# Optimization experiments

Measured on AMD Instinct MI355X. Metric: run time of the kernel, lower is better.

## Reference

```python
import jax, jax.numpy as jnp
import numpy as np

B = 1; IMG = 256; P = 16; INC = 3; C = 384; NH = 12; HD = C // NH
WS = 8; SH = WS // 2; HP = IMG // P; L = HP * HP; NW = (HP // WS) ** 2
NB = 12; OC = 4; EPS = 1e-5; MLP = 4 * C


def _rel_index(w):
    coords = np.stack(np.meshgrid(np.arange(w), np.arange(w), indexing='ij'))
    cf = coords.reshape(2, -1)
    rel = (cf[:, :, None] - cf[:, None, :]).transpose(1, 2, 0)
    rel[:, :, 0] += w - 1
    rel[:, :, 1] += w - 1
    rel[:, :, 0] *= 2 * w - 1
    return rel.sum(-1)  # (w*w, w*w)


def _attn_mask():
    m = np.zeros((HP, HP))
    cnt = 0
    for hs in (slice(0, -WS), slice(-WS, -SH), slice(-SH, None)):
        for ws_ in (slice(0, -WS), slice(-WS, -SH), slice(-SH, None)):
            m[hs, ws_] = cnt
            cnt += 1
    mw = m.reshape(HP // WS, WS, HP // WS, WS).transpose(0, 2, 1, 3).reshape(-1, WS * WS)
    d = mw[:, None, :] - mw[:, :, None]
    return np.where(d != 0, -100.0, 0.0).astype(np.float32)  # (NW, 64, 64)

_REL_IDX = jnp.asarray(_rel_index(WS))
_AMASK = jnp.asarray(_attn_mask())


def _ln(x, w, b):
    m = jnp.mean(x, -1, keepdims=True)
    d = x - m
    v = jnp.mean(d * d, -1, keepdims=True)
    return d * jax.lax.rsqrt(v + EPS) * w + b


def _resize_ac(x, oh, ow):
    # bilinear, align_corners=True
    H, W = x.shape[-2], x.shape[-1]
    def idx(o, n):
        s = jnp.linspace(0.0, n - 1.0, o)
        i0 = jnp.floor(s).astype(jnp.int32)
        i1 = jnp.minimum(i0 + 1, n - 1)
        return i0, i1, (s - i0.astype(s.dtype)).astype(x.dtype)
    y0, y1, wy = idx(oh, H)
    x0, x1, wx = idx(ow, W)
    r = x[..., y0, :] * (1 - wy)[:, None] + x[..., y1, :] * wy[:, None]
    return r[..., x0] * (1 - wx) + r[..., x1] * wx


def setup_inputs():
    key = jax.random.key(0)
    ks = jax.random.split(key, 16)
    f32 = jnp.float32
    def rn(k, shape, s=0.02):
        return jax.random.normal(k, shape, dtype=f32) * s
    return {
        'x': jax.random.normal(ks[0], (B, INC, IMG, IMG), f32),
        'patch_w': rn(ks[1], (C, INC, P, P), 0.05),
        'patch_b': jnp.zeros((C,), f32),
        'pos_embed': rn(ks[2], (1, L, C)),
        'ln1_w': jnp.ones((NB, C), f32), 'ln1_b': jnp.zeros((NB, C), f32),
        'qkv_w': rn(ks[3], (NB, 3 * C, C)),
        'proj_w': rn(ks[4], (NB, C, C)), 'proj_b': jnp.zeros((NB, C), f32),
        'rpb': rn(ks[5], (NB, (2 * WS - 1) ** 2, NH)),
        'ln2_w': jnp.ones((NB, C), f32), 'ln2_b': jnp.zeros((NB, C), f32),
        'fc1_w': rn(ks[6], (NB, MLP, C)), 'fc1_b': jnp.zeros((NB, MLP), f32),
        'fc2_w': rn(ks[7], (NB, C, MLP)), 'fc2_b': jnp.zeros((NB, C), f32),
        'skip_w': rn(ks[8], (OC, C), 0.05), 'skip_b': jnp.zeros((OC,), f32),
        'dt1_w': rn(ks[9], (C, INC, P, P), 0.05), 'dt1_b': jnp.zeros((INC,), f32),
        'bn1_w': jnp.ones((INC,), f32), 'bn1_b': jnp.zeros((INC,), f32),
        'dt2_w': rn(ks[10], (INC, OC, P, P), 0.05), 'dt2_b': jnp.zeros((OC,), f32),
        'bn2_w': jnp.ones((OC,), f32), 'bn2_b': jnp.zeros((OC,), f32),
    }


def reference(x, patch_w, patch_b, pos_embed, ln1_w, ln1_b, qkv_w, proj_w, proj_b,
              rpb, ln2_w, ln2_b, fc1_w, fc1_b, fc2_w, fc2_b, skip_w, skip_b,
              dt1_w, dt1_b, bn1_w, bn1_b, dt2_w, dt2_b, bn2_w, bn2_b):
    scale = HD ** -0.5
    # --- patch embed (conv k=P, s=P) ---
    xr = x.reshape(B, INC, HP, P, HP, P)
    f = jnp.einsum('bchpwq,ocpq->bohw', xr, patch_w) + patch_b[None, :, None, None]
    # --- buggy token flatten, replicated exactly from the source ---
    t = jnp.transpose(f.reshape(B, C, P, HP // P, P, HP // P), (0, 3, 5, 1, 2, 4)).reshape(B, L, C)
    t = t + pos_embed

    def block(h, p):
        l1w, l1b, qw, pw, pb, rt, l2w, l2b, f1w, f1b, f2w, f2b = p
        sc = h
        y = _ln(h, l1w, l1b).reshape(B, HP, HP, C)
        y = jnp.roll(y, (-SH, -SH), axis=(1, 2))  # every block is shifted in this model
        yw = y.reshape(B, HP // WS, WS, HP // WS, WS, C).transpose(0, 1, 3, 2, 4, 5)
        yw = yw.reshape(B * NW, WS * WS, C)
        qkv = (yw @ qw.T).reshape(B * NW, WS * WS, 3, NH, HD).transpose(2, 0, 3, 1, 4)
        q, k, v = qkv[0], qkv[1], qkv[2]
        attn = jnp.einsum('wnid,wnjd->wnij', q, k) * scale
        bias = rt[_REL_IDX].transpose(2, 0, 1)  # (NH, 64, 64)
        attn = attn + bias[None]
        attn = attn.reshape(B, NW, NH, WS * WS, WS * WS) + _AMASK[None, :, None]
        attn = jax.nn.softmax(attn.reshape(B * NW, NH, WS * WS, WS * WS), axis=-1)
        o = jnp.einsum('wnij,wnjd->wnid', attn, v).transpose(0, 2, 1, 3).reshape(B * NW, WS * WS, C)
        o = o @ pw.T + pb
        o = o.reshape(B, HP // WS, HP // WS, WS, WS, C).transpose(0, 1, 3, 2, 4, 5).reshape(B, HP, HP, C)
        o = jnp.roll(o, (SH, SH), axis=(1, 2)).reshape(B, L, C)
        h = sc + o
        z = _ln(h, l2w, l2b)
        z = jax.nn.gelu(z @ f1w.T + f1b, approximate=False)
        h = h + (z @ f2w.T + f2b)
        return h, None

    t, _ = jax.lax.scan(block, t, (ln1_w, ln1_b, qkv_w, proj_w, proj_b, rpb,
                                   ln2_w, ln2_b, fc1_w, fc1_b, fc2_w, fc2_b))

    f = t.reshape(B, HP, HP, C).transpose(0, 3, 1, 2)  # (B, C, 16, 16)
    # --- decoder ---
    skip = jnp.einsum('bchw,oc->bohw', f, skip_w) + skip_b[None, :, None, None]
    # interpolate(skip, size=(H, W)) with H, W == skip's own size: identity.
    d = jnp.einsum('bchw,cokl->bohkwl', f, dt1_w).reshape(B, INC, HP * P, HP * P) + dt1_b[None, :, None, None]
    d = jax.nn.relu(d / jnp.sqrt(1.0 + EPS) * bn1_w[None, :, None, None] + bn1_b[None, :, None, None])
    d = jnp.einsum('bchw,cokl->bohkwl', d, dt2_w).reshape(B, OC, HP * P * P, HP * P * P) + dt2_b[None, :, None, None]
    d = d / jnp.sqrt(1.0 + EPS) * bn2_w[None, :, None, None] + bn2_b[None, :, None, None]
    # Upsample(scale_factor = IMG // (P*P) = 1): identity.
    skip_up = _resize_ac(skip, d.shape[2], d.shape[3])
    out = (d + skip_up).reshape(B, -1, IMG, IMG)
    return out
```

## Files before the change

### kernel.cpp

```cpp
#include <hip/hip_runtime.h>
#include <cmath>

typedef _Float16 v8h __attribute__((ext_vector_type(8)));
typedef float v4f __attribute__((ext_vector_type(4)));

#define DEV __device__ __forceinline__

DEV int win_map(int m) {
  int w = m >> 6, tok = m & 63;
  int r = ((w >> 1) * 8 + (tok >> 3) + 4) & 15;
  int c = ((w & 1) * 8 + (tok & 7) + 4) & 15;
  return r * 16 + c;
}

template<int MAP>
DEV float4 loadA4(const float* __restrict__ A, int m, int k, int K) {
  if constexpr (MAP == 0) {
    return *(const float4*)(A + (size_t)m * K + k);
  } else if constexpr (MAP == 1) {
    return *(const float4*)(A + (size_t)win_map(m) * 384 + k);
  } else {
    int h = m >> 4, w = m & 15;
    int inc = k >> 8, rem = k & 255, p = rem >> 4, q = rem & 15;
    return *(const float4*)(A + inc * 65536 + (h * 16 + p) * 256 + w * 16 + q);
  }
}

template<int WAVES_M, int WAVES_N, int WN, int MAP, bool LN, int EPI>
__launch_bounds__(256)
__global__ void mgemm(const float* __restrict__ A, const float* __restrict__ W,
                      const float* __restrict__ bias,
                      const float* __restrict__ lnw, const float* __restrict__ lnb,
                      const float* __restrict__ resid, const float* __restrict__ aux,
                      float* __restrict__ Cout, int N, int K) {
  constexpr int BM = WAVES_M * 16;
  constexpr int BN = WAVES_N * WN * 16;
  constexpr int BK = 64;
  constexpr int BKP = BK + 8;

  __shared__ _Float16 As[BM][BKP];
  __shared__ _Float16 Ws[BN][BKP];
  __shared__ float redS[256], redQ[256];
  __shared__ float lmean[BM], lrstd[BM];

  const int t = threadIdx.x;
  const int wave = t >> 6, lane = t & 63;
  const int m0 = blockIdx.y * BM, n0 = blockIdx.x * BN;

  if constexpr (LN) {
    constexpr int PARTS = 256 / BM;
    int r = t / PARTS, part = t % PARTS;
    int chunk = K / PARTS;
    float s = 0.f, sq = 0.f;
    for (int k = part * chunk; k < (part + 1) * chunk; k += 4) {
      float4 v = loadA4<MAP>(A, m0 + r, k, K);
      s += v.x + v.y + v.z + v.w;
      sq += v.x * v.x + v.y * v.y + v.z * v.z + v.w * v.w;
    }
    redS[t] = s; redQ[t] = sq;
    __syncthreads();
    if (t < BM) {
      float ss = 0.f, qq = 0.f;
      for (int p = 0; p < PARTS; ++p) { ss += redS[t * PARTS + p]; qq += redQ[t * PARTS + p]; }
      float mean = ss / K;
      float var = qq / K - mean * mean;
      lmean[t] = mean;
      lrstd[t] = rsqrtf(var + 1e-5f);
    }
    __syncthreads();
  }

  const int wm = wave % WAVES_M;
  const int wn = wave / WAVES_M;
  const int mBase = wm * 16;
  const int nBase = wn * (WN * 16);

  v4f acc[WN] = {};

  for (int k0 = 0; k0 < K; k0 += BK) {
    constexpr int AREP = (BM * 16) / 256;
#pragma unroll
    for (int i = 0; i < AREP; ++i) {
      int idx = t + i * 256;
      int row = idx >> 4;
      int kc = (idx & 15) * 4;
      float4 v = loadA4<MAP>(A, m0 + row, k0 + kc, K);
      if constexpr (LN) {
        float4 lw = *(const float4*)(lnw + k0 + kc);
        float4 lb = *(const float4*)(lnb + k0 + kc);
        float mu = lmean[row], rs = lrstd[row];
        v.x = (v.x - mu) * rs * lw.x + lb.x;
        v.y = (v.y - mu) * rs * lw.y + lb.y;
        v.z = (v.z - mu) * rs * lw.z + lb.z;
        v.w = (v.w - mu) * rs * lw.w + lb.w;
      }
      _Float16* dst = &As[row][kc];
      dst[0] = (_Float16)v.x; dst[1] = (_Float16)v.y;
      dst[2] = (_Float16)v.z; dst[3] = (_Float16)v.w;
    }
    constexpr int WREP = (BN * 16) / 256;
#pragma unroll
    for (int i = 0; i < WREP; ++i) {
      int idx = t + i * 256;
      int row = idx >> 4;
      int kc = (idx & 15) * 4;
      float4 v = *(const float4*)(W + (size_t)(n0 + row) * K + k0 + kc);
      _Float16* dst = &Ws[row][kc];
      dst[0] = (_Float16)v.x; dst[1] = (_Float16)v.y;
      dst[2] = (_Float16)v.z; dst[3] = (_Float16)v.w;
    }
    __syncthreads();
#pragma unroll
    for (int kk = 0; kk < BK; kk += 32) {
      v8h af = *(const v8h*)&As[mBase + (lane & 15)][kk + (lane >> 4) * 8];
#pragma unroll
      for (int nt = 0; nt < WN; ++nt) {
        v8h bf = *(const v8h*)&Ws[nBase + nt * 16 + (lane & 15)][kk + (lane >> 4) * 8];
        acc[nt] = __builtin_amdgcn_mfma_f32_16x16x32_f16(af, bf, acc[nt], 0, 0, 0);
      }
    }
    __syncthreads();
  }

  const int quad = lane >> 4;
  const int col = lane & 15;
#pragma unroll
  for (int nt = 0; nt < WN; ++nt) {
    int n = n0 + nBase + nt * 16 + col;
#pragma unroll
    for (int r = 0; r < 4; ++r) {
      int m = m0 + mBase + quad * 4 + r;
      float v = acc[nt][r];
      if constexpr (EPI == 0) {
        Cout[(size_t)m * N + n] = v;
      } else if constexpr (EPI == 1) {
        Cout[(size_t)m * N + n] = resid[(size_t)m * N + n] + v + bias[n];
      } else if constexpr (EPI == 2) {
        float z = v + bias[n];
        Cout[(size_t)m * N + n] = 0.5f * z * (1.0f + erff(z * 0.70710678118654752f));
      } else {
        Cout[n * 256 + m] = v + bias[n] + aux[n * 256 + m];
      }
    }
  }
}

__launch_bounds__(256)
__global__ void attn_k(const float* __restrict__ qkv, const float* __restrict__ rpb,
                       float* __restrict__ obuf) {
  __shared__ float qs[64][33], ks[64][33], vs[64][33];
  __shared__ float ps[64][68];
  __shared__ float rbias[225];
  __shared__ int labv[64];
  const int t = threadIdx.x;
  const int w = blockIdx.x & 3, head = blockIdx.x >> 2;

  for (int idx = t; idx < 2048; idx += 256) {
    int tok = idx >> 5, d = idx & 31;
    int base = (w * 64 + tok) * 1152 + head * 32 + d;
    qs[tok][d] = qkv[base];
    ks[tok][d] = qkv[base + 384];
    vs[tok][d] = qkv[base + 768];
  }
  for (int idx = t; idx < 225; idx += 256) rbias[idx] = rpb[idx * 12 + head];
  if (t < 64) {
    int r = (w >> 1) * 8 + (t >> 3), c = (w & 1) * 8 + (t & 7);
    int lr = r < 8 ? 0 : (r < 12 ? 1 : 2);
    int lc = c < 8 ? 0 : (c < 12 ? 1 : 2);
    labv[t] = lr * 3 + lc;
  }
  __syncthreads();

  const int tx = t & 15, ty = t >> 4;
  float acc[4][4] = {};
  for (int d = 0; d < 32; ++d) {
    float a[4], b[4];
#pragma unroll
    for (int ii = 0; ii < 4; ++ii) a[ii] = qs[ty * 4 + ii][d];
#pragma unroll
    for (int jj = 0; jj < 4; ++jj) b[jj] = ks[tx * 4 + jj][d];
#pragma unroll
    for (int ii = 0; ii < 4; ++ii)
#pragma unroll
      for (int jj = 0; jj < 4; ++jj) acc[ii][jj] += a[ii] * b[jj];
  }
  const float scale = 0.17677669529663687f;
#pragma unroll
  for (int ii = 0; ii < 4; ++ii) {
    int i = ty * 4 + ii;
    int yi = i >> 3, xi = i & 7, li = labv[i];
    float pv[4];
    float mx = -1e30f;
#pragma unroll
    for (int jj = 0; jj < 4; ++jj) {
      int j = tx * 4 + jj;
      int yj = j >> 3, xj = j & 7;
      int ri = (yi - yj + 7) * 15 + (xi - xj + 7);
      float s = acc[ii][jj] * scale + rbias[ri] + (li == labv[j] ? 0.f : -100.f);
      pv[jj] = s;
      mx = fmaxf(mx, s);
    }
    for (int off = 1; off < 16; off <<= 1) mx = fmaxf(mx, __shfl_xor(mx, off));
    float sum = 0.f;
#pragma unroll
    for (int jj = 0; jj < 4; ++jj) { pv[jj] = expf(pv[jj] - mx); sum += pv[jj]; }
    for (int off = 1; off < 16; off <<= 1) sum += __shfl_xor(sum, off);
    float inv = 1.0f / sum;
#pragma unroll
    for (int jj = 0; jj < 4; ++jj) ps[i][tx * 4 + jj] = pv[jj] * inv;
  }
  __syncthreads();

  float o2[4][2] = {};
  for (int j = 0; j < 64; ++j) {
    float v0 = vs[j][tx * 2 + 0], v1 = vs[j][tx * 2 + 1];
#pragma unroll
    for (int ii = 0; ii < 4; ++ii) {
      float p = ps[ty * 4 + ii][j];
      o2[ii][0] += p * v0;
      o2[ii][1] += p * v1;
    }
  }
#pragma unroll
  for (int ii = 0; ii < 4; ++ii) {
    int l = win_map(w * 64 + ty * 4 + ii);
    obuf[l * 384 + head * 32 + tx * 2 + 0] = o2[ii][0];
    obuf[l * 384 + head * 32 + tx * 2 + 1] = o2[ii][1];
  }
}

__global__ void skip_k(const float* __restrict__ hfin, const float* __restrict__ sw,
                       const float* __restrict__ sb, float* __restrict__ skipb) {
  int o = blockIdx.x, t = threadIdx.x;
  float acc = 0.f;
  for (int c = 0; c < 384; ++c) acc += hfin[t * 384 + c] * sw[o * 384 + c];
  skipb[o * 256 + t] = acc + sb[o];
}

__global__ void d1_k(const float* __restrict__ hfin, const float* __restrict__ wgt,
                     const float* __restrict__ bvec, const float* __restrict__ bnw,
                     const float* __restrict__ bnb, float* __restrict__ d1) {
  __shared__ float hs[2][384];
  const int t = threadIdx.x;
  const int l0 = blockIdx.x * 2;
  for (int idx = t; idx < 768; idx += 256) {
    int pi = idx / 384, c = idx % 384;
    hs[pi][c] = hfin[(l0 + pi) * 384 + c];
  }
  __syncthreads();
  const float invs = rsqrtf(1.0f + 1e-5f);
  const int kk = t >> 4, ll = t & 15;
  for (int o = 0; o < 3; ++o) {
    float a0 = 0.f, a1 = 0.f;
    for (int c = 0; c < 384; ++c) {
      float wv = wgt[c * 768 + o * 256 + t];
      a0 += hs[0][c] * wv;
      a1 += hs[1][c] * wv;
    }
    float sw = bnw[o] * invs, bb = bvec[o], sb = bnb[o];
    float v0 = fmaxf((a0 + bb) * sw + sb, 0.f);
    float v1 = fmaxf((a1 + bb) * sw + sb, 0.f);
#pragma unroll
    for (int pi = 0; pi < 2; ++pi) {
      int l = l0 + pi;
      int h = l >> 4, wq = l & 15;
      float v = pi ? v1 : v0;
      d1[o * 65536 + (h * 16 + kk) * 256 + (wq * 16 + ll)] = v;
    }
  }
}

__launch_bounds__(256)
__global__ void d2_k(const float* __restrict__ d1, const float* __restrict__ w2,
                     const float* __restrict__ b2, const float* __restrict__ bnw,
                     const float* __restrict__ bnb, const float* __restrict__ skipb,
                     float* __restrict__ out) {
  __shared__ float d1s[3][256];
  __shared__ float wcol[3][16];
  __shared__ float srow[16];
  const int t = threadIdx.x;
  const int y = blockIdx.x, o = blockIdx.y;
  const int h2 = y >> 4, k = y & 15;
  for (int idx = t; idx < 768; idx += 256) {
    int c = idx >> 8, wi = idx & 255;
    d1s[c][wi] = d1[c * 65536 + h2 * 256 + wi];
  }
  if (t < 48) {
    int c = t >> 4, l2 = t & 15;
    wcol[c][l2] = w2[c * 1024 + o * 256 + k * 16 + l2];
  }
  if (t < 16) {
    const float dy = 15.0f / 4095.0f;
    float s = y * dy;
    int y0 = min((int)s, 15);
    int y1 = min(y0 + 1, 15);
    float wy = s - (float)y0;
    float a0 = skipb[o * 256 + y0 * 16 + t];
    float a1 = skipb[o * 256 + y1 * 16 + t];
    srow[t] = a0 + (a1 - a0) * wy;
  }
  __syncthreads();
  const float invs = rsqrtf(1.0f + 1e-5f);
  const float sw = bnw[o] * invs;
  const float base = b2[o] * sw + bnb[o];
  const float dx = 15.0f / 4095.0f;
  const size_t obase = ((size_t)o << 24) + ((size_t)y << 12);
#pragma unroll
  for (int rep = 0; rep < 4; ++rep) {
    int x4 = t + rep * 256;
    int x = x4 * 4;
    int wi = x >> 4;
    int l2b = x & 15;
    float vals[4];
#pragma unroll
    for (int e = 0; e < 4; ++e) {
      int l2 = l2b + e;
      float v = d1s[0][wi] * wcol[0][l2] + d1s[1][wi] * wcol[1][l2] + d1s[2][wi] * wcol[2][l2];
      v = v * sw + base;
      float s = (float)(x + e) * dx;
      int x0 = min((int)s, 15);
      int x1 = min(x0 + 1, 15);
      float wx = s - (float)x0;
      vals[e] = v + srow[x0] + (srow[x1] - srow[x0]) * wx;
    }
    *(float4*)&out[obase + x] = make_float4(vals[0], vals[1], vals[2], vals[3]);
  }
}

extern "C" void kernel_launch(void* const* d_in, const int* in_sizes, int n_in,
                              void* d_out, int out_size, void* d_ws, size_t ws_size,
                              hipStream_t stream) {
  const float* x       = (const float*)d_in[0];
  const float* patch_w = (const float*)d_in[1];
  const float* patch_b = (const float*)d_in[2];
  const float* pos     = (const float*)d_in[3];
  const float* ln1w    = (const float*)d_in[4];
  const float* ln1b    = (const float*)d_in[5];
  const float* qkvw    = (const float*)d_in[6];
  const float* projw   = (const float*)d_in[7];
  const float* projb   = (const float*)d_in[8];
  const float* rpb     = (const float*)d_in[9];
  const float* ln2w    = (const float*)d_in[10];
  const float* ln2b    = (const float*)d_in[11];
  const float* fc1w    = (const float*)d_in[12];
  const float* fc1b    = (const float*)d_in[13];
  const float* fc2w    = (const float*)d_in[14];
  const float* fc2b    = (const float*)d_in[15];
  const float* skipw   = (const float*)d_in[16];
  const float* skipbi  = (const float*)d_in[17];
  const float* dt1w    = (const float*)d_in[18];
  const float* dt1b    = (const float*)d_in[19];
  const float* bn1w    = (const float*)d_in[20];
  const float* bn1b    = (const float*)d_in[21];
  const float* dt2w    = (const float*)d_in[22];
  const float* dt2b    = (const float*)d_in[23];
  const float* bn2w    = (const float*)d_in[24];
  const float* bn2b    = (const float*)d_in[25];
  float* out = (float*)d_out;
  float* ws = (float*)d_ws;

  float* h    = ws;
  float* qkvb = ws + 98304;
  float* obuf = ws + 393216;
  float* zb   = ws + 491520;
  float* d1b  = ws + 884736;
  float* skb  = ws + 1081344;

  mgemm<2, 2, 2, 2, false, 3><<<dim3(6, 8), 256, 0, stream>>>(
      x, patch_w, patch_b, nullptr, nullptr, nullptr, pos, h, 384, 768);

  for (int b = 0; b < 12; ++b) {
    mgemm<2, 2, 2, 1, true, 0><<<dim3(18, 8), 256, 0, stream>>>(
        h, qkvw + (size_t)b * 442368, nullptr, ln1w + b * 384, ln1b + b * 384,
        nullptr, nullptr, qkvb, 1152, 384);
    attn_k<<<48, 256, 0, stream>>>(qkvb, rpb + b * 2700, obuf);
    mgemm<1, 4, 1, 0, false, 1><<<dim3(6, 16), 256, 0, stream>>>(
        obuf, projw + (size_t)b * 147456, projb + b * 384, nullptr, nullptr,
        h, nullptr, h, 384, 384);
    mgemm<2, 2, 2, 0, true, 2><<<dim3(24, 8), 256, 0, stream>>>(
        h, fc1w + (size_t)b * 589824, fc1b + b * 1536, ln2w + b * 384, ln2b + b * 384,
        nullptr, nullptr, zb, 1536, 384);
    mgemm<1, 4, 1, 0, false, 1><<<dim3(6, 16), 256, 0, stream>>>(
        zb, fc2w + (size_t)b * 589824, fc2b + b * 384, nullptr, nullptr,
        h, nullptr, h, 384, 1536);
  }

  skip_k<<<4, 256, 0, stream>>>(h, skipw, skipbi, skb);
  d1_k<<<128, 256, 0, stream>>>(h, dt1w, dt1b, bn1w, bn1b, d1b);
  d2_k<<<dim3(4096, 4), 256, 0, stream>>>(d1b, dt2w, dt2b, bn2w, bn2b, skb, out);
}
```

Before: 1.408 ms.

## Fuse whole forward pass into one persistent kernel with grid barriers

Replaces the sequence of roughly 65 separate kernel launches (patch embed, per-block GEMMs and attention, decoder) with a single persistent kernel of 256 workgroups. Stages are separated by a software grid barrier built on atomics. Each stage loops over its tiles with a grid stride, and shared memory is a union across stages. The intent is to remove launch overhead and inter-kernel gaps, which dominate for these small GEMMs. The cost is atomic spin-wait barriers, with a deadlock risk if all 256 workgroups are not co-resident, and fewer parallel blocks in the large decoder stage.

```diff
diff --git a/kernel.cpp b/kernel.cpp
--- a/kernel.cpp
+++ b/kernel.cpp
@@ -5,6 +5,8 @@
 typedef float v4f __attribute__((ext_vector_type(4)));
 
 #define DEV __device__ __forceinline__
+
+constexpr int NWG = 256;
 
 DEV int win_map(int m) {
   int w = m >> 6, tok = m & 63;
@@ -26,366 +28,436 @@
   }
 }
 
+union SMem {
+  struct {
+    _Float16 As[32][72];
+    _Float16 Ws[64][72];
+    float redS[256], redQ[256];
+    float lmean[32], lrstd[32];
+  } g;
+  struct {
+    float qs[64][33], ks[64][33], vs[64][33];
+    float ps[64][68];
+    float rbias[225];
+    int labv[64];
+  } at;
+  struct { float hs[2][384]; } d1;
+  struct { float d1s[3][256]; float wcol[3][16]; float srow[16]; } d2;
+};
+
+DEV void gridbar(unsigned* cnt, unsigned* flag, unsigned& gen) {
+  __syncthreads();
+  if (threadIdx.x == 0) {
+    __threadfence();
+    unsigned target = ++gen;
+    unsigned prev = __hip_atomic_fetch_add(cnt, 1u, __ATOMIC_ACQ_REL, __HIP_MEMORY_SCOPE_AGENT);
+    if (prev == NWG - 1) {
+      __hip_atomic_store(cnt, 0u, __ATOMIC_RELAXED, __HIP_MEMORY_SCOPE_AGENT);
+      __hip_atomic_store(flag, target, __ATOMIC_RELEASE, __HIP_MEMORY_SCOPE_AGENT);
+    } else {
+      while (__hip_atomic_load(flag, __ATOMIC_RELAXED, __HIP_MEMORY_SCOPE_AGENT) < target)
+        __builtin_amdgcn_s_sleep(2);
+    }
+    __threadfence();
+  }
+  __syncthreads();
+}
+
 template<int WAVES_M, int WAVES_N, int WN, int MAP, bool LN, int EPI>
-__launch_bounds__(256)
-__global__ void mgemm(const float* __restrict__ A, const float* __restrict__ W,
-                      const float* __restrict__ bias,
-                      const float* __restrict__ lnw, const float* __restrict__ lnb,
-                      const float* __restrict__ resid, const float* __restrict__ aux,
-                      float* __restrict__ Cout, int N, int K) {
+DEV void gemm_stage(SMem& sm, const float* __restrict__ A, const float* __restrict__ W,
+                    const float* __restrict__ bias,
+                    const float* __restrict__ lnw, const float* __restrict__ lnb,
+                    const float* __restrict__ resid, const float* __restrict__ aux,
+                    float* __restrict__ Cout, int N, int K) {
   constexpr int BM = WAVES_M * 16;
   constexpr int BN = WAVES_N * WN * 16;
   constexpr int BK = 64;
-  constexpr int BKP = BK + 8;
-
-  __shared__ _Float16 As[BM][BKP];
-  __shared__ _Float16 Ws[BN][BKP];
-  __shared__ float redS[256], redQ[256];
-  __shared__ float lmean[BM], lrstd[BM];
+  static_assert(BM <= 32 && BN <= 64, "SMem capacity");
+  auto& As = sm.g.As;
+  auto& Ws = sm.g.Ws;
 
   const int t = threadIdx.x;
   const int wave = t >> 6, lane = t & 63;
-  const int m0 = blockIdx.y * BM, n0 = blockIdx.x * BN;
-
-  if constexpr (LN) {
-    constexpr int PARTS = 256 / BM;
-    int r = t / PARTS, part = t % PARTS;
-    int chunk = K / PARTS;
-    float s = 0.f, sq = 0.f;
-    for (int k = part * chunk; k < (part + 1) * chunk; k += 4) {
-      float4 v = loadA4<MAP>(A, m0 + r, k, K);
-      s += v.x + v.y + v.z + v.w;
-      sq += v.x * v.x + v.y * v.y + v.z * v.z + v.w * v.w;
-    }
-    redS[t] = s; redQ[t] = sq;
-    __syncthreads();
-    if (t < BM) {
-      float ss = 0.f, qq = 0.f;
-      for (int p = 0; p < PARTS; ++p) { ss += redS[t * PARTS + p]; qq += redQ[t * PARTS + p]; }
-      float mean = ss / K;
-      float var = qq / K - mean * mean;
-      lmean[t] = mean;
-      lrstd[t] = rsqrtf(var + 1e-5f);
-    }
-    __syncthreads();
-  }
-
   const int wm = wave % WAVES_M;
   const int wn = wave / WAVES_M;
   const int mBase = wm * 16;
   const int nBase = wn * (WN * 16);
-
-  v4f acc[WN] = {};
-
-  for (int k0 = 0; k0 < K; k0 += BK) {
-    constexpr int AREP = (BM * 16) / 256;
-#pragma unroll
-    for (int i = 0; i < AREP; ++i) {
-      int idx = t + i * 256;
-      int row = idx >> 4;
-      int kc = (idx & 15) * 4;
-      float4 v = loadA4<MAP>(A, m0 + row, k0 + kc, K);
-      if constexpr (LN) {
-        float4 lw = *(const float4*)(lnw + k0 + kc);
-        float4 lb = *(const float4*)(lnb + k0 + kc);
-        float mu = lmean[row], rs = lrstd[row];
-        v.x = (v.x - mu) * rs * lw.x + lb.x;
-        v.y = (v.y - mu) * rs * lw.y + lb.y;
-        v.z = (v.z - mu) * rs * lw.z + lb.z;
-        v.w = (v.w - mu) * rs * lw.w + lb.w;
-      }
-      _Float16* dst = &As[row][kc];
-      dst[0] = (_Float16)v.x; dst[1] = (_Float16)v.y;
-      dst[2] = (_Float16)v.z; dst[3] = (_Float16)v.w;
-    }
-    constexpr int WREP = (BN * 16) / 256;
-#pragma unroll
-    for (int i = 0; i < WREP; ++i) {
-      int idx = t + i * 256;
-      int row = idx >> 4;
-      int kc = (idx & 15) * 4;
-      float4 v = *(const float4*)(W + (size_t)(n0 + row) * K + k0 + kc);
-      _Float16* dst = &Ws[row][kc];
-      dst[0] = (_Float16)v.x; dst[1] = (_Float16)v.y;
-      dst[2] = (_Float16)v.z; dst[3] = (_Float16)v.w;
-    }
-    __syncthreads();
-#pragma unroll
-    for (int kk = 0; kk < BK; kk += 32) {
-      v8h af = *(const v8h*)&As[mBase + (lane & 15)][kk + (lane >> 4) * 8];
-#pragma unroll
-      for (int nt = 0; nt < WN; ++nt) {
-        v8h bf = *(const v8h*)&Ws[nBase + nt * 16 + (lane & 15)][kk + (lane >> 4) * 8];
-        acc[nt] = __builtin_amdgcn_mfma_f32_16x16x32_f16(af, bf, acc[nt], 0, 0, 0);
-      }
-    }
-    __syncthreads();
-  }
-
-  const int quad = lane >> 4;
-  const int col = lane & 15;
-#pragma unroll
-  for (int nt = 0; nt < WN; ++nt) {
-    int n = n0 + nBase + nt * 16 + col;
-#pragma unroll
-    for (int r = 0; r < 4; ++r) {
-      int m = m0 + mBase + quad * 4 + r;
-      float v = acc[nt][r];
-      if constexpr (EPI == 0) {
-        Cout[(size_t)m * N + n] = v;
-      } else if constexpr (EPI == 1) {
-        Cout[(size_t)m * N + n] = resid[(size_t)m * N + n] + v + bias[n];
-      } else if constexpr (EPI == 2) {
-        float z = v + bias[n];
-        Cout[(size_t)m * N + n] = 0.5f * z * (1.0f + erff(z * 0.70710678118654752f));
-      } else {
-        Cout[n * 256 + m] = v + bias[n] + aux[n * 256 + m];
-      }
-    }
-  }
-}
+  const int tilesX = N / BN;
+  const int tiles = tilesX * (256 / BM);
+
+  for (int tile = blockIdx.x; tile < tiles; tile += NWG) {
+    const int m0 = (tile / tilesX) * BM;
+    const int n0 = (tile % tilesX) * BN;
+
+    if constexpr (LN) {
+      constexpr int PARTS = 256 / BM;
+      int r = t / PARTS, part = t % PARTS;
+      int chunk = K / PARTS;
+      float s = 0.f, sq = 0.f;
+      for (int k = part * chunk; k < (part + 1) * chunk; k += 4) {
+        float4 v = loadA4<MAP>(A, m0 + r, k, K);
+        s += v.x + v.y + v.z + v.w;
+        sq += v.x * v.x + v.y * v.y + v.z * v.z + v.w * v.w;
+      }
+      sm.g.redS[t] = s; sm.g.redQ[t] = sq;
+      __syncthreads();
+      if (t < BM) {
+        float ss = 0.f, qq = 0.f;
+        for (int p2 = 0; p2 < PARTS; ++p2) { ss += sm.g.redS[t * PARTS + p2]; qq += sm.g.redQ[t * PARTS + p2]; }
+        float mean = ss / K;
+        float var = qq / K - mean * mean;
+        sm.g.lmean[t] = mean;
+        sm.g.lrstd[t] = rsqrtf(var + 1e-5f);
+      }
+      __syncthreads();
+    }
+
+    v4f acc[WN] = {};
+
+    for (int k0 = 0; k0 < K; k0 += BK) {
+      constexpr int AREP = (BM * 16) / 256;
+#pragma unroll
+      for (int i = 0; i < AREP; ++i) {
+        int idx = t + i * 256;
+        int row = idx >> 4;
+        int kc = (idx & 15) * 4;
+        float4 v = loadA4<MAP>(A, m0 + row, k0 + kc, K);
+        if constexpr (LN) {
+          float4 lw = *(const float4*)(lnw + k0 + kc);
+          float4 lb = *(const float4*)(lnb + k0 + kc);
+          float mu = sm.g.lmean[row], rs = sm.g.lrstd[row];
+          v.x = (v.x - mu) * rs * lw.x + lb.x;
+          v.y = (v.y - mu) * rs * lw.y + lb.y;
+          v.z = (v.z - mu) * rs * lw.z + lb.z;
+          v.w = (v.w - mu) * rs * lw.w + lb.w;
+        }
+        _Float16* dst = &As[row][kc];
+        dst[0] = (_Float16)v.x; dst[1] = (_Float16)v.y;
+        dst[2] = (_Float16)v.z; dst[3] = (_Float16)v.w;
+      }
+      constexpr int WREP = (BN * 16) / 256;
+#pragma unroll
+      for (int i = 0; i < WREP; ++i) {
+        int idx = t + i * 256;
+        int row = idx >> 4;
+        int kc = (idx & 15) * 4;
+        float4 v = *(const float4*)(W + (size_t)(n0 + row) * K + k0 + kc);
+        _Float16* dst = &Ws[row][kc];
+        dst[0] = (_Float16)v.x; dst[1] = (_Float16)v.y;
+        dst[2] = (_Float16)v.z; dst[3] = (_Float16)v.w;
+      }
+      __syncthreads();
+#pragma unroll
+      for (int kk = 0; kk < BK; kk += 32) {
+        v8h af = *(const v8h*)&As[mBase + (lane & 15)][kk + (lane >> 4) * 8];
+#pragma unroll
+        for (int nt = 0; nt < WN; ++nt) {
+          v8h bf = *(const v8h*)&Ws[nBase + nt * 16 + (lane & 15)][kk + (lane >> 4) * 8];
+          acc[nt] = __builtin_amdgcn_mfma_f32_16x16x32_f16(af, bf, acc[nt], 0, 0, 0);
+        }
+      }
+      __syncthreads();
+    }
+
+    const int quad = lane >> 4;
+    const int col = lane & 15;
+#pragma unroll
+    for (int nt = 0; nt < WN; ++nt) {
+      int n = n0 + nBase + nt * 16 + col;
+#pragma unroll
+      for (int r2 = 0; r2 < 4; ++r2) {
+        int m = m0 + mBase + quad * 4 + r2;
+        float v = acc[nt][r2];
+        if constexpr (EPI == 0) {
+          Cout[(size_t)m * N + n] = v;
+        } else if constexpr (EPI == 1) {
+          Cout[(size_t)m * N + n] = resid[(size_t)m * N + n] + v + bias[n];
+        } else if constexpr (EPI == 2) {
+          float z = v + bias[n];
+          Cout[(size_t)m * N + n] = 0.5f * z * (1.0f + erff(z * 0.70710678118654752f));
+        } else {
+          Cout[n * 256 + m] = v + bias[n] + aux[n * 256 + m];
+        }
+      }
+    }
+  }
+}
+
+DEV void attn_stage(SMem& sm, const float* __restrict__ qkv, const float* __restrict__ rpb,
+                    float* __restrict__ obuf) {
+  const int t = threadIdx.x;
+  for (int u = blockIdx.x; u < 48; u += NWG) {
+    const int w = u & 3, head = u >> 2;
+
+    for (int idx = t; idx < 2048; idx += 256) {
+      int tok = idx >> 5, d = idx & 31;
+      int base = (w * 64 + tok) * 1152 + head * 32 + d;
+      sm.at.qs[tok][d] = qkv[base];
+      sm.at.ks[tok][d] = qkv[base + 384];
+      sm.at.vs[tok][d] = qkv[base + 768];
+    }
+    for (int idx = t; idx < 225; idx += 256) sm.at.rbias[idx] = rpb[idx * 12 + head];
+    if (t < 64) {
+      int r = (w >> 1) * 8 + (t >> 3), c = (w & 1) * 8 + (t & 7);
+      int lr = r < 8 ? 0 : (r < 12 ? 1 : 2);
+      int lc = c < 8 ? 0 : (c < 12 ? 1 : 2);
+      sm.at.labv[t] = lr * 3 + lc;
+    }
+    __syncthreads();
+
+    const int tx = t & 15, ty = t >> 4;
+    float acc[4][4] = {};
+    for (int d = 0; d < 32; ++d) {
+      float a[4], b[4];
+#pragma unroll
+      for (int ii = 0; ii < 4; ++ii) a[ii] = sm.at.qs[ty * 4 + ii][d];
+#pragma unroll
+      for (int jj = 0; jj < 4; ++jj) b[jj] = sm.at.ks[tx * 4 + jj][d];
+#pragma unroll
+      for (int ii = 0; ii < 4; ++ii)
+#pragma unroll
+        for (int jj = 0; jj < 4; ++jj) acc[ii][jj] += a[ii] * b[jj];
+    }
+    const float scale = 0.17677669529663687f;
+#pragma unroll
+    for (int ii = 0; ii < 4; ++ii) {
+      int i = ty * 4 + ii;
+      int yi = i >> 3, xi = i & 7, li = sm.at.labv[i];
+      float pv[4];
+      float mx = -1e30f;
+#pragma unroll
+      for (int jj = 0; jj < 4; ++jj) {
+        int j = tx * 4 + jj;
+        int yj = j >> 3, xj = j & 7;
+        int ri = (yi - yj + 7) * 15 + (xi - xj + 7);
+        float s = acc[ii][jj] * scale + sm.at.rbias[ri] + (li == sm.at.labv[j] ? 0.f : -100.f);
+        pv[jj] = s;
+        mx = fmaxf(mx, s);
+      }
+      for (int off = 1; off < 16; off <<= 1) mx = fmaxf(mx, __shfl_xor(mx, off));
+      float sum = 0.f;
+#pragma unroll
+      for (int jj = 0; jj < 4; ++jj) { pv[jj] = expf(pv[jj] - mx); sum += pv[jj]; }
+      for (int off = 1; off < 16; off <<= 1) sum += __shfl_xor(sum, off);
+      float inv = 1.0f / sum;
+#pragma unroll
+      for (int jj = 0; jj < 4; ++jj) sm.at.ps[i][tx * 4 + jj] = pv[jj] * inv;
+    }
+    __syncthreads();
+
+    float o2[4][2] = {};
+    for (int j = 0; j < 64; ++j) {
+      float v0 = sm.at.vs[j][tx * 2 + 0], v1 = sm.at.vs[j][tx * 2 + 1];
+#pragma unroll
+      for (int ii = 0; ii < 4; ++ii) {
+        float p = sm.at.ps[ty * 4 + ii][j];
+        o2[ii][0] += p * v0;
+        o2[ii][1] += p * v1;
+      }
+    }
+#pragma unroll
+    for (int ii = 0; ii < 4; ++ii) {
+      int l = win_map(w * 64 + ty * 4 + ii);
+      obuf[l * 384 + head * 32 + tx * 2 + 0] = o2[ii][0];
+      obuf[l * 384 + head * 32 + tx * 2 + 1] = o2[ii][1];
+    }
+    __syncthreads();
+  }
+}
+
+DEV void dec1_stage(SMem& sm, const float* __restrict__ hfin,
+                    const float* __restrict__ wgt, const float* __restrict__ bvec,
+                    const float* __restrict__ bnw, const float* __restrict__ bnb,
+                    float* __restrict__ d1,
+                    const float* __restrict__ sw, const float* __restrict__ sb,
+                    float* __restrict__ skipb) {
+  const int t = threadIdx.x;
+  const int wg = blockIdx.x;
+  if (wg < 128) {
+    const int l0 = wg * 2;
+    for (int idx = t; idx < 768; idx += 256) {
+      int pi = idx / 384, c = idx % 384;
+      sm.d1.hs[pi][c] = hfin[(l0 + pi) * 384 + c];
+    }
+    __syncthreads();
+    const float invs = rsqrtf(1.0f + 1e-5f);
+    const int kk = t >> 4, ll = t & 15;
+    for (int o = 0; o < 3; ++o) {
+      float a0 = 0.f, a1 = 0.f;
+      for (int c = 0; c < 384; ++c) {
+        float wv = wgt[c * 768 + o * 256 + t];
+        a0 += sm.d1.hs[0][c] * wv;
+        a1 += sm.d1.hs[1][c] * wv;
+      }
+      float swv = bnw[o] * invs, bb = bvec[o], sbv = bnb[o];
+      float v0 = fmaxf((a0 + bb) * swv + sbv, 0.f);
+      float v1 = fmaxf((a1 + bb) * swv + sbv, 0.f);
+#pragma unroll
+      for (int pi = 0; pi < 2; ++pi) {
+        int l = l0 + pi;
+        int hh = l >> 4, wq = l & 15;
+        d1[o * 65536 + (hh * 16 + kk) * 256 + (wq * 16 + ll)] = pi ? v1 : v0;
+      }
+    }
+  } else if (wg < 132) {
+    const int o = wg - 128;
+    float acc = 0.f;
+    for (int c = 0; c < 384; ++c) acc += hfin[t * 384 + c] * sw[o * 384 + c];
+    skipb[o * 256 + t] = acc + sb[o];
+  }
+}
+
+DEV void dec2_stage(SMem& sm, const float* __restrict__ d1, const float* __restrict__ w2,
+                    const float* __restrict__ b2, const float* __restrict__ bnw,
+                    const float* __restrict__ bnb, const float* __restrict__ skipb,
+                    float* __restrict__ out) {
+  const int t = threadIdx.x;
+  for (int u = blockIdx.x; u < 16384; u += NWG) {
+    const int y = u & 4095, o = u >> 12;
+    const int h2 = y >> 4, k = y & 15;
+    for (int idx = t; idx < 768; idx += 256) {
+      int c = idx >> 8, wi = idx & 255;
+      sm.d2.d1s[c][wi] = d1[c * 65536 + h2 * 256 + wi];
+    }
+    if (t < 48) {
+      int c = t >> 4, l2 = t & 15;
+      sm.d2.wcol[c][l2] = w2[c * 1024 + o * 256 + k * 16 + l2];
+    }
+    if (t < 16) {
+      const float dy = 15.0f / 4095.0f;
+      float s = y * dy;
+      int y0 = min((int)s, 15);
+      int y1 = min(y0 + 1, 15);
+      float wy = s - (float)y0;
+      float a0 = skipb[o * 256 + y0 * 16 + t];
+      float a1 = skipb[o * 256 + y1 * 16 + t];
+      sm.d2.srow[t] = a0 + (a1 - a0) * wy;
+    }
+    __syncthreads();
+    const float invs = rsqrtf(1.0f + 1e-5f);
+    const float swv = bnw[o] * invs;
+    const float base = b2[o] * swv + bnb[o];
+    const float dx = 15.0f / 4095.0f;
+    const size_t obase = ((size_t)o << 24) + ((size_t)y << 12);
+#pragma unroll
+    for (int rep = 0; rep < 4; ++rep) {
+      int x4 = t + rep * 256;
+      int x = x4 * 4;
+      int wi = x >> 4;
+      int l2b = x & 15;
+      float vals[4];
+#pragma unroll
+      for (int e = 0; e < 4; ++e) {
+        int l2 = l2b + e;
+        float v = sm.d2.d1s[0][wi] * sm.d2.wcol[0][l2] + sm.d2.d1s[1][wi] * sm.d2.wcol[1][l2] +
+                  sm.d2.d1s[2][wi] * sm.d2.wcol[2][l2];
+        v = v * swv + base;
+        float s = (float)(x + e) * dx;
+        int x0 = min((int)s, 15);
+        int x1 = min(x0 + 1, 15);
+        float wx = s - (float)x0;
+        vals[e] = v + sm.d2.srow[x0] + (sm.d2.srow[x1] - sm.d2.srow[x0]) * wx;
+      }
+      *(float4*)&out[obase + x] = make_float4(vals[0], vals[1], vals[2], vals[3]);
+    }
+    __syncthreads();
+  }
+}
+
+struct MegaP {
+  const float *x, *patch_w, *patch_b, *pos;
+  const float *ln1w, *ln1b, *qkvw, *projw, *projb, *rpb, *ln2w, *ln2b;
+  const float *fc1w, *fc1b, *fc2w, *fc2b;
+  const float *skipw, *skipbi, *dt1w, *dt1b, *bn1w, *bn1b, *dt2w, *dt2b, *bn2w, *bn2b;
+  float *out, *ws;
+  unsigned *cnt, *flag;
+};
 
 __launch_bounds__(256)
-__global__ void attn_k(const float* __restrict__ qkv, const float* __restrict__ rpb,
-                       float* __restrict__ obuf) {
-  __shared__ float qs[64][33], ks[64][33], vs[64][33];
-  __shared__ float ps[64][68];
-  __shared__ float rbias[225];
-  __shared__ int labv[64];
-  const int t = threadIdx.x;
-  const int w = blockIdx.x & 3, head = blockIdx.x >> 2;
-
-  for (int idx = t; idx < 2048; idx += 256) {
-    int tok = idx >> 5, d = idx & 31;
-    int base = (w * 64 + tok) * 1152 + head * 32 + d;
-    qs[tok][d] = qkv[base];
-    ks[tok][d] = qkv[base + 384];
-    vs[tok][d] = qkv[base + 768];
-  }
-  for (int idx = t; idx < 225; idx += 256) rbias[idx] = rpb[idx * 12 + head];
-  if (t < 64) {
-    int r = (w >> 1) * 8 + (t >> 3), c = (w & 1) * 8 + (t & 7);
-    int lr = r < 8 ? 0 : (r < 12 ? 1 : 2);
-    int lc = c < 8 ? 0 : (c < 12 ? 1 : 2);
-    labv[t] = lr * 3 + lc;
-  }
-  __syncthreads();
-
-  const int tx = t & 15, ty = t >> 4;
-  float acc[4][4] = {};
-  for (int d = 0; d < 32; ++d) {
-    float a[4], b[4];
-#pragma unroll
-    for (int ii = 0; ii < 4; ++ii) a[ii] = qs[ty * 4 + ii][d];
-#pragma unroll
-    for (int jj = 0; jj < 4; ++jj) b[jj] = ks[tx * 4 + jj][d];
-#pragma unroll
-    for (int ii = 0; ii < 4; ++ii)
-#pragma unroll
-      for (int jj = 0; jj < 4; ++jj) acc[ii][jj] += a[ii] * b[jj];
-  }
-  const float scale = 0.17677669529663687f;
-#pragma unroll
-  for (int ii = 0; ii < 4; ++ii) {
-    int i = ty * 4 + ii;
-    int yi = i >> 3, xi = i & 7, li = labv[i];
-    float pv[4];
-    float mx = -1e30f;
-#pragma unroll
-    for (int jj = 0; jj < 4; ++jj) {
-      int j = tx * 4 + jj;
-      int yj = j >> 3, xj = j & 7;
-      int ri = (yi - yj + 7) * 15 + (xi - xj + 7);
-      float s = acc[ii][jj] * scale + rbias[ri] + (li == labv[j] ? 0.f : -100.f);
-      pv[jj] = s;
-      mx = fmaxf(mx, s);
-    }
-    for (int off = 1; off < 16; off <<= 1) mx = fmaxf(mx, __shfl_xor(mx, off));
-    float sum = 0.f;
-#pragma unroll
-    for (int jj = 0; jj < 4; ++jj) { pv[jj] = expf(pv[jj] - mx); sum += pv[jj]; }
-    for (int off = 1; off < 16; off <<= 1) sum += __shfl_xor(sum, off);
-    float inv = 1.0f / sum;
-#pragma unroll
-    for (int jj = 0; jj < 4; ++jj) ps[i][tx * 4 + jj] = pv[jj] * inv;
-  }
-  __syncthreads();
-
-  float o2[4][2] = {};
-  for (int j = 0; j < 64; ++j) {
-    float v0 = vs[j][tx * 2 + 0], v1 = vs[j][tx * 2 + 1];
-#pragma unroll
-    for (int ii = 0; ii < 4; ++ii) {
-      float p = ps[ty * 4 + ii][j];
-      o2[ii][0] += p * v0;
-      o2[ii][1] += p * v1;
-    }
-  }
-#pragma unroll
-  for (int ii = 0; ii < 4; ++ii) {
-    int l = win_map(w * 64 + ty * 4 + ii);
-    obuf[l * 384 + head * 32 + tx * 2 + 0] = o2[ii][0];
-    obuf[l * 384 + head * 32 + tx * 2 + 1] = o2[ii][1];
-  }
-}
-
-__global__ void skip_k(const float* __restrict__ hfin, const float* __restrict__ sw,
-                       const float* __restrict__ sb, float* __restrict__ skipb) {
-  int o = blockIdx.x, t = threadIdx.x;
-  float acc = 0.f;
-  for (int c = 0; c < 384; ++c) acc += hfin[t * 384 + c] * sw[o * 384 + c];
-  skipb[o * 256 + t] = acc + sb[o];
-}
-
-__global__ void d1_k(const float* __restrict__ hfin, const float* __restrict__ wgt,
-                     const float* __restrict__ bvec, const float* __restrict__ bnw,
-                     const float* __restrict__ bnb, float* __restrict__ d1) {
-  __shared__ float hs[2][384];
-  const int t = threadIdx.x;
-  const int l0 = blockIdx.x * 2;
-  for (int idx = t; idx < 768; idx += 256) {
-    int pi = idx / 384, c = idx % 384;
-    hs[pi][c] = hfin[(l0 + pi) * 384 + c];
-  }
-  __syncthreads();
-  const float invs = rsqrtf(1.0f + 1e-5f);
-  const int kk = t >> 4, ll = t & 15;
-  for (int o = 0; o < 3; ++o) {
-    float a0 = 0.f, a1 = 0.f;
-    for (int c = 0; c < 384; ++c) {
-      float wv = wgt[c * 768 + o * 256 + t];
-      a0 += hs[0][c] * wv;
-      a1 += hs[1][c] * wv;
-    }
-    float sw = bnw[o] * invs, bb = bvec[o], sb = bnb[o];
-    float v0 = fmaxf((a0 + bb) * sw + sb, 0.f);
-    float v1 = fmaxf((a1 + bb) * sw + sb, 0.f);
-#pragma unroll
-    for (int pi = 0; pi < 2; ++pi) {
-      int l = l0 + pi;
-      int h = l >> 4, wq = l & 15;
-      float v = pi ? v1 : v0;
-      d1[o * 65536 + (h * 16 + kk) * 256 + (wq * 16 + ll)] = v;
-    }
-  }
-}
-
-__launch_bounds__(256)
-__global__ void d2_k(const float* __restrict__ d1, const float* __restrict__ w2,
-                     const float* __restrict__ b2, const float* __restrict__ bnw,
-                     const float* __restrict__ bnb, const float* __restrict__ skipb,
-                     float* __restrict__ out) {
-  __shared__ float d1s[3][256];
-  __shared__ float wcol[3][16];
-  __shared__ float srow[16];
-  const int t = threadIdx.x;
-  const int y = blockIdx.x, o = blockIdx.y;
-  const int h2 = y >> 4, k = y & 15;
-  for (int idx = t; idx < 768; idx += 256) {
-    int c = idx >> 8, wi = idx & 255;
-    d1s[c][wi] = d1[c * 65536 + h2 * 256 + wi];
-  }
-  if (t < 48) {
-    int c = t >> 4, l2 = t & 15;
-    wcol[c][l2] = w2[c * 1024 + o * 256 + k * 16 + l2];
-  }
-  if (t < 16) {
-    const float dy = 15.0f / 4095.0f;
-    float s = y * dy;
-    int y0 = min((int)s, 15);
-    int y1 = min(y0 + 1, 15);
-    float wy = s - (float)y0;
-    float a0 = skipb[o * 256 + y0 * 16 + t];
-    float a1 = skipb[o * 256 + y1 * 16 + t];
-    srow[t] = a0 + (a1 - a0) * wy;
-  }
-  __syncthreads();
-  const float invs = rsqrtf(1.0f + 1e-5f);
-  const float sw = bnw[o] * invs;
-  const float base = b2[o] * sw + bnb[o];
-  const float dx = 15.0f / 4095.0f;
-  const size_t obase = ((size_t)o << 24) + ((size_t)y << 12);
-#pragma unroll
-  for (int rep = 0; rep < 4; ++rep) {
-    int x4 = t + rep * 256;
-    int x = x4 * 4;
-    int wi = x >> 4;
-    int l2b = x & 15;
-    float vals[4];
-#pragma unroll
-    for (int e = 0; e < 4; ++e) {
-      int l2 = l2b + e;
-      float v = d1s[0][wi] * wcol[0][l2] + d1s[1][wi] * wcol[1][l2] + d1s[2][wi] * wcol[2][l2];
-      v = v * sw + base;
-      float s = (float)(x + e) * dx;
-      int x0 = min((int)s, 15);
-      int x1 = min(x0 + 1, 15);
-      float wx = s - (float)x0;
-      vals[e] = v + srow[x0] + (srow[x1] - srow[x0]) * wx;
-    }
-    *(float4*)&out[obase + x] = make_float4(vals[0], vals[1], vals[2], vals[3]);
-  }
+__global__ void swin_mega(MegaP p) {
+  __shared__ SMem sm;
+  unsigned gen = 0;
+
+  float* h    = p.ws;
+  float* qkvb = p.ws + 98304;
+  float* obuf = p.ws + 393216;
+  float* zb   = p.ws + 491520;
+  float* d1b  = p.ws + 884736;
+  float* skb  = p.ws + 1081344;
+
+  gemm_stage<2, 2, 2, 2, false, 3>(sm, p.x, p.patch_w, p.patch_b, nullptr, nullptr,
+                                   nullptr, p.pos, h, 384, 768);
+  gridbar(p.cnt, p.flag, gen);
+
+#pragma unroll 1
+  for (int b = 0; b < 12; ++b) {
+    gemm_stage<2, 2, 2, 1, true, 0>(sm, h, p.qkvw + (size_t)b * 442368, nullptr,
+                                    p.ln1w + b * 384, p.ln1b + b * 384,
+                                    nullptr, nullptr, qkvb, 1152, 384);
+    gridbar(p.cnt, p.flag, gen);
+    attn_stage(sm, qkvb, p.rpb + b * 2700, obuf);
+    gridbar(p.cnt, p.flag, gen);
+    gemm_stage<1, 4, 1, 0, false, 1>(sm, obuf, p.projw + (size_t)b * 147456,
+                                     p.projb + b * 384, nullptr, nullptr,
+                                     h, nullptr, h, 384, 384);
+    gridbar(p.cnt, p.flag, gen);
+    gemm_stage<2, 2, 2, 0, true, 2>(sm, h, p.fc1w + (size_t)b * 589824,
+                                    p.fc1b + b * 1536, p.ln2w + b * 384, p.ln2b + b * 384,
+                                    nullptr, nullptr, zb, 1536, 384);
+    gridbar(p.cnt, p.flag, gen);
+    gemm_stage<1, 4, 1, 0, false, 1>(sm, zb, p.fc2w + (size_t)b * 589824,
+                                     p.fc2b + b * 384, nullptr, nullptr,
+                                     h, nullptr, h, 384, 1536);
+    gridbar(p.cnt, p.flag, gen);
+  }
+
+  dec1_stage(sm, h, p.dt1w, p.dt1b, p.bn1w, p.bn1b, d1b, p.skipw, p.skipbi, skb);
+  gridbar(p.cnt, p.flag, gen);
+  dec2_stage(sm, d1b, p.dt2w, p.dt2b, p.bn2w, p.bn2b, skb, p.out);
+}
+
+__global__ void init_bar_k(unsigned* bar) {
+  if (threadIdx.x < 96) bar[threadIdx.x] = 0;
 }
 
 extern "C" void kernel_launch(void* const* d_in, const int* in_sizes, int n_in,
                               void* d_out, int out_size, void* d_ws, size_t ws_size,
                               hipStream_t stream) {
-  const float* x       = (const float*)d_in[0];
-  const float* patch_w = (const float*)d_in[1];
-  const float* patch_b = (const float*)d_in[2];
-  const float* pos     = (const float*)d_in[3];
-  const float* ln1w    = (const float*)d_in[4];
-  const float* ln1b    = (const float*)d_in[5];
-  const float* qkvw    = (const float*)d_in[6];
-  const float* projw   = (const float*)d_in[7];
-  const float* projb   = (const float*)d_in[8];
-  const float* rpb     = (const float*)d_in[9];
-  const float* ln2w    = (const float*)d_in[10];
-  const float* ln2b    = (const float*)d_in[11];
-  const float* fc1w    = (const float*)d_in[12];
-  const float* fc1b    = (const float*)d_in[13];
-  const float* fc2w    = (const float*)d_in[14];
-  const float* fc2b    = (const float*)d_in[15];
-  const float* skipw   = (const float*)d_in[16];
-  const float* skipbi  = (const float*)d_in[17];
-  const float* dt1w    = (const float*)d_in[18];
-  const float* dt1b    = (const float*)d_in[19];
-  const float* bn1w    = (const float*)d_in[20];
-  const float* bn1b    = (const float*)d_in[21];
-  const float* dt2w    = (const float*)d_in[22];
-  const float* dt2b    = (const float*)d_in[23];
-  const float* bn2w    = (const float*)d_in[24];
-  const float* bn2b    = (const float*)d_in[25];
-  float* out = (float*)d_out;
   float* ws = (float*)d_ws;
-
-  float* h    = ws;
-  float* qkvb = ws + 98304;
-  float* obuf = ws + 393216;
-  float* zb   = ws + 491520;
-  float* d1b  = ws + 884736;
-  float* skb  = ws + 1081344;
-
-  mgemm<2, 2, 2, 2, false, 3><<<dim3(6, 8), 256, 0, stream>>>(
-      x, patch_w, patch_b, nullptr, nullptr, nullptr, pos, h, 384, 768);
-
-  for (int b = 0; b < 12; ++b) {
-    mgemm<2, 2, 2, 1, true, 0><<<dim3(18, 8), 256, 0, stream>>>(
-        h, qkvw + (size_t)b * 442368, nullptr, ln1w + b * 384, ln1b + b * 384,
-        nullptr, nullptr, qkvb, 1152, 384);
-    attn_k<<<48, 256, 0, stream>>>(qkvb, rpb + b * 2700, obuf);
-    mgemm<1, 4, 1, 0, false, 1><<<dim3(6, 16), 256, 0, stream>>>(
-        obuf, projw + (size_t)b * 147456, projb + b * 384, nullptr, nullptr,
-        h, nullptr, h, 384, 384);
-    mgemm<2, 2, 2, 0, true, 2><<<dim3(24, 8), 256, 0, stream>>>(
-        h, fc1w + (size_t)b * 589824, fc1b + b * 1536, ln2w + b * 384, ln2b + b * 384,
-        nullptr, nullptr, zb, 1536, 384);
-    mgemm<1, 4, 1, 0, false, 1><<<dim3(6, 16), 256, 0, stream>>>(
-        zb, fc2w + (size_t)b * 589824, fc2b + b * 384, nullptr, nullptr,
-        h, nullptr, h, 384, 1536);
-  }
-
-  skip_k<<<4, 256, 0, stream>>>(h, skipw, skipbi, skb);
-  d1_k<<<128, 256, 0, stream>>>(h, dt1w, dt1b, bn1w, bn1b, d1b);
-  d2_k<<<dim3(4096, 4), 256, 0, stream>>>(d1b, dt2w, dt2b, bn2w, bn2b, skb, out);
-}
+  unsigned* bar = (unsigned*)(ws + 1082368);
+
+  MegaP p;
+  p.x       = (const float*)d_in[0];
+  p.patch_w = (const float*)d_in[1];
+  p.patch_b = (const float*)d_in[2];
+  p.pos     = (const float*)d_in[3];
+  p.ln1w    = (const float*)d_in[4];
+  p.ln1b    = (const float*)d_in[5];
+  p.qkvw    = (const float*)d_in[6];
+  p.projw   = (const float*)d_in[7];
+  p.projb   = (const float*)d_in[8];
+  p.rpb     = (const float*)d_in[9];
+  p.ln2w    = (const float*)d_in[10];
+  p.ln2b    = (const float*)d_in[11];
+  p.fc1w    = (const float*)d_in[12];
+  p.fc1b    = (const float*)d_in[13];
+  p.fc2w    = (const float*)d_in[14];
+  p.fc2b    = (const float*)d_in[15];
+  p.skipw   = (const float*)d_in[16];
+  p.skipbi  = (const float*)d_in[17];
+  p.dt1w    = (const float*)d_in[18];
+  p.dt1b    = (const float*)d_in[19];
+  p.bn1w    = (const float*)d_in[20];
+  p.bn1b    = (const float*)d_in[21];
+  p.dt2w    = (const float*)d_in[22];
+  p.dt2b    = (const float*)d_in[23];
+  p.bn2w    = (const float*)d_in[24];
+  p.bn2b    = (const float*)d_in[25];
+  p.out = (float*)d_out;
+  p.ws  = ws;
+  p.cnt  = bar;
+  p.flag = bar + 64;
+
+  init_bar_k<<<1, 128, 0, stream>>>(bar);
+  swin_mega<<<NWG, 256, 0, stream>>>(p);
+}
```

Measured after the change: 2.086 ms. 1.48x slower.
